# Optimization experiments

Hardware: AMD Instinct MI355X
Metric: run time of the kernel (lower is better)

## Reference

```python
import jax, jax.numpy as jnp
import numpy as np

NEG_SLOPE = 0.2  # PyG GATConv default


def gat_conv(x, edge_index, W, a_src, a_dst, bias):
    """Single-head PyG-style GATConv (eval mode, add_self_loops=True)."""
    N = x.shape[0]
    h = x @ W  # [N, F_out]
    # add self loops
    loops = jnp.arange(N, dtype=edge_index.dtype)
    src = jnp.concatenate([edge_index[0], loops])  # [E+N]
    dst = jnp.concatenate([edge_index[1], loops])
    # per-edge attention logits: a_src . h_j + a_dst . h_i  (j=src, i=dst)
    alpha_s = h @ a_src  # [N]
    alpha_d = h @ a_dst  # [N]
    e = jax.nn.leaky_relu(alpha_s[src] + alpha_d[dst], NEG_SLOPE)  # [E+N]
    # segment softmax over incoming edges of each dst node
    m = jax.ops.segment_max(e, dst, num_segments=N)
    ex = jnp.exp(e - m[dst])
    denom = jax.ops.segment_sum(ex, dst, num_segments=N)
    alpha = ex / denom[dst]  # [E+N]
    # weighted scatter-aggregate of source features
    out = jax.ops.segment_sum(h[src] * alpha[:, None], dst, num_segments=N)
    return out + bias


def setup_inputs() -> dict:
    key = jax.random.key(0)
    ks = jax.random.split(key, 12)
    N, E = 100000, 3200000
    Fin, H, Fout = 128, 32, 32
    x = jax.random.normal(ks[0], (N, Fin), dtype=jnp.float32)
    edge_index = jax.random.randint(ks[1], (2, E), 0, N, dtype=jnp.int64)
    s = 1.0 / np.sqrt(Fin)
    W1 = jax.random.uniform(ks[2], (Fin, H), jnp.float32, -s, s)
    a1s = jax.random.uniform(ks[3], (H,), jnp.float32, -s, s)
    a1d = jax.random.uniform(ks[4], (H,), jnp.float32, -s, s)
    b1 = jnp.zeros((H,), jnp.float32)
    s2 = 1.0 / np.sqrt(H)
    W2 = jax.random.uniform(ks[5], (H, H), jnp.float32, -s2, s2)
    a2s = jax.random.uniform(ks[6], (H,), jnp.float32, -s2, s2)
    a2d = jax.random.uniform(ks[7], (H,), jnp.float32, -s2, s2)
    b2 = jnp.zeros((H,), jnp.float32)
    Wf = jax.random.uniform(ks[8], (H, Fout), jnp.float32, -s2, s2)
    bf = jax.random.uniform(ks[9], (Fout,), jnp.float32, -s2, s2)
    return {"x": x, "edge_index": edge_index, "W1": W1, "a1s": a1s, "a1d": a1d,
            "b1": b1, "W2": W2, "a2s": a2s, "a2d": a2d, "b2": b2,
            "Wf": Wf, "bf": bf}


def reference(x, edge_index, W1, a1s, a1d, b1, W2, a2s, a2d, b2, Wf, bf):
    h = jax.nn.relu(gat_conv(x, edge_index, W1, a1s, a1d, b1))
    h = jax.nn.relu(gat_conv(h, edge_index, W2, a2s, a2d, b2))
    return h @ Wf + bf
```

## Files before the change

kernel.cpp:

```cpp
#include <hip/hip_runtime.h>

#define NEG_SLOPE 0.2f
#define BK_LOG 9
#define BK_NODES (1 << BK_LOG)
#define TILE_EPT 24
#define TILE_E (256 * TILE_EPT)

typedef __attribute__((ext_vector_type(8))) short bf8_t;
typedef __attribute__((ext_vector_type(4))) float f32x4;

__device__ __forceinline__ float leaky(float v) { return v > 0.0f ? v : NEG_SLOPE * v; }

__device__ __forceinline__ unsigned short f2bf(float f) {
    unsigned u = __float_as_uint(f);
    u += 0x7fffu + ((u >> 16) & 1u);
    return (unsigned short)(u >> 16);
}
__device__ __forceinline__ float bf2f(unsigned short h) {
    return __uint_as_float(((unsigned)h) << 16);
}

__device__ __forceinline__ int scan256_excl(int v, int* tmp) {
    int t = threadIdx.x;
    tmp[t] = v;
    __syncthreads();
    for (int d = 1; d < 256; d <<= 1) {
        int x = (t >= d) ? tmp[t - d] : 0;
        __syncthreads();
        tmp[t] += x;
        __syncthreads();
    }
    int r = tmp[t] - v;
    __syncthreads();
    return r;
}


__global__ __launch_bounds__(256) void k_bzero(int* __restrict__ bcnt) {
    bcnt[threadIdx.x] = 0;
}

__global__ __launch_bounds__(256) void k_bcount(const int* __restrict__ edst,
                                                int* __restrict__ bcnt, int E) {
    __shared__ int th[256];
    int t = threadIdx.x;
    th[t] = 0;
    __syncthreads();
    int base = blockIdx.x * TILE_E;
#pragma unroll
    for (int k = 0; k < TILE_EPT; ++k) {
        int e = base + t + k * 256;
        if (e < E) atomicAdd(&th[edst[e] >> BK_LOG], 1);
    }
    __syncthreads();
    if (th[t]) atomicAdd(&bcnt[t], th[t]);
}

__global__ __launch_bounds__(256) void k_bscan(const int* __restrict__ bcnt,
                                               int* __restrict__ bbase,
                                               int* __restrict__ bcur,
                                               int* __restrict__ off, int N, int E) {
    __shared__ int tmp[256];
    int t = threadIdx.x;
    int ex = scan256_excl(bcnt[t], tmp);
    bbase[t] = ex;
    bcur[t]  = ex;
    if (t == 0) { bbase[256] = E; off[N] = E; }
}

__global__ __launch_bounds__(256) void k_bplace(const int* __restrict__ esrc,
                                                const int* __restrict__ edst,
                                                int* __restrict__ bcur,
                                                unsigned* __restrict__ pairs, int E) {
    __shared__ int2 sp[TILE_E];
    __shared__ int th[256], tx[256], rb[256], tmp[256];
    int t = threadIdx.x;
    th[t] = 0;
    __syncthreads();
    int base = blockIdx.x * TILE_E;
    int tot  = min(TILE_E, E - base);
#pragma unroll
    for (int k = 0; k < TILE_EPT; ++k) {
        int e = base + t + k * 256;
        if (e < E) atomicAdd(&th[edst[e] >> BK_LOG], 1);
    }
    __syncthreads();
    int cnt = th[t];
    tx[t] = scan256_excl(cnt, tmp);
    rb[t] = atomicAdd(&bcur[t], cnt);
    th[t] = 0;
    __syncthreads();
#pragma unroll
    for (int k = 0; k < TILE_EPT; ++k) {
        int e = base + t + k * 256;
        if (e < E) {
            int s = esrc[e], d = edst[e];
            int b = d >> BK_LOG;
            int r = atomicAdd(&th[b], 1);
            sp[tx[b] + r] = make_int2(s, d);
        }
    }
    __syncthreads();
    for (int i = t; i < tot; i += 256) {
        int2 p = sp[i];
        int  b = p.y >> BK_LOG;
        pairs[rb[b] + (i - tx[b])] =
            ((unsigned)p.x << BK_LOG) | (unsigned)(p.y & (BK_NODES - 1));
    }
}

__global__ __launch_bounds__(512) void k_csr(const int* __restrict__ bbase,
                                             const unsigned* __restrict__ pairs,
                                             int* __restrict__ off,
                                             int* __restrict__ csr, int N) {
    __shared__ int lh[BK_NODES], lx[BK_NODES];
    int b = blockIdx.x, t = threadIdx.x;
    int lo = bbase[b], hi = bbase[b + 1];
    int node0 = b << BK_LOG;
    lh[t] = 0;
    __syncthreads();
    for (int j = lo + t; j < hi; j += 512)
        atomicAdd(&lh[pairs[j] & (BK_NODES - 1)], 1);
    __syncthreads();
    lx[t] = lh[t];
    __syncthreads();
    for (int d = 1; d < BK_NODES; d <<= 1) {
        int x0 = (t >= d) ? lx[t - d] : 0;
        __syncthreads();
        lx[t] += x0;
        __syncthreads();
    }
    lx[t] -= lh[t];
    if (node0 + t < N) off[node0 + t] = lo + lx[t];
    lh[t] = 0;
    __syncthreads();
    for (int j = lo + t; j < hi; j += 512) {
        unsigned p  = pairs[j];
        int      li = p & (BK_NODES - 1);
        int      r  = atomicAdd(&lh[li], 1);
        csr[lo + lx[li] + r] = (int)(p >> BK_LOG);
    }
}

__global__ __launch_bounds__(256) void k_wsplit(const float* __restrict__ W,
                                                unsigned short* __restrict__ wh,
                                                unsigned short* __restrict__ wl,
                                                int K) {
    int idx = blockIdx.x * 256 + threadIdx.x;
    int KT = K >> 5;
    if (idx >= KT * 128) return;
    int lane = idx & 63;
    int nt = (idx >> 6) & 1;
    int kt = idx >> 7;
    int q = lane >> 4, c = lane & 15;
#pragma unroll
    for (int j = 0; j < 8; ++j) {
        int k = kt * 32 + q * 8 + j;
        int n = nt * 16 + c;
        float w = W[k * 32 + n];
        unsigned short hi = f2bf(w);
        wh[idx * 8 + j] = hi;
        wl[idx * 8 + j] = f2bf(w - bf2f(hi));
    }
}

template <int FIN, bool ATT>
__global__ __launch_bounds__(256) void gemm_mfma(
    const float* __restrict__ x,
    const unsigned short* __restrict__ wh, const unsigned short* __restrict__ wl,
    const float* __restrict__ a_s, const float* __restrict__ a_d,
    const float* __restrict__ bias,
    float* __restrict__ h, float* __restrict__ alpha_s,
    float* __restrict__ alpha_d, int N)
{
    constexpr int KT = FIN / 32;
    int lane = threadIdx.x & 63;
    int mt   = blockIdx.x * 4 + (threadIdx.x >> 6);
    int m0   = mt * 16;
    if (m0 >= N) return;
    int q = lane >> 4, c = lane & 15;

    bf8_t Bh[KT][2], Bl[KT][2];
#pragma unroll
    for (int kt = 0; kt < KT; ++kt)
#pragma unroll
        for (int nt = 0; nt < 2; ++nt) {
            Bh[kt][nt] = *(const bf8_t*)(wh + ((size_t)(kt * 2 + nt) * 64 + lane) * 8);
            Bl[kt][nt] = *(const bf8_t*)(wl + ((size_t)(kt * 2 + nt) * 64 + lane) * 8);
        }

    int rowa = m0 + c;
    if (rowa >= N) rowa = N - 1;
    const float* xr = x + (size_t)rowa * FIN;
    bf8_t Ah[KT], Al[KT];
#pragma unroll
    for (int kt = 0; kt < KT; ++kt) {
        f32x4 v0 = *(const f32x4*)(xr + kt * 32 + q * 8);
        f32x4 v1 = *(const f32x4*)(xr + kt * 32 + q * 8 + 4);
#pragma unroll
        for (int j = 0; j < 8; ++j) {
            float f = (j < 4) ? v0[j] : v1[j - 4];
            unsigned short hi = f2bf(f);
            Ah[kt][j] = (short)hi;
            Al[kt][j] = (short)f2bf(f - bf2f(hi));
        }
    }

    f32x4 acc0 = {0.f, 0.f, 0.f, 0.f}, acc1 = {0.f, 0.f, 0.f, 0.f};
#pragma unroll
    for (int kt = 0; kt < KT; ++kt) {
        acc0 = __builtin_amdgcn_mfma_f32_16x16x32_bf16(Ah[kt], Bh[kt][0], acc0, 0, 0, 0);
        acc1 = __builtin_amdgcn_mfma_f32_16x16x32_bf16(Ah[kt], Bh[kt][1], acc1, 0, 0, 0);
        acc0 = __builtin_amdgcn_mfma_f32_16x16x32_bf16(Al[kt], Bh[kt][0], acc0, 0, 0, 0);
        acc1 = __builtin_amdgcn_mfma_f32_16x16x32_bf16(Al[kt], Bh[kt][1], acc1, 0, 0, 0);
        acc0 = __builtin_amdgcn_mfma_f32_16x16x32_bf16(Ah[kt], Bl[kt][0], acc0, 0, 0, 0);
        acc1 = __builtin_amdgcn_mfma_f32_16x16x32_bf16(Ah[kt], Bl[kt][1], acc1, 0, 0, 0);
    }

#pragma unroll
    for (int reg = 0; reg < 4; ++reg) {
        int r = m0 + q * 4 + reg;
        if (r < N) {
            float v0s = acc0[reg], v1s = acc1[reg];
            if (!ATT) { v0s += bias[c]; v1s += bias[c + 16]; }
            h[(size_t)r * 32 + c]      = v0s;
            h[(size_t)r * 32 + 16 + c] = v1s;
        }
    }
    if (ATT) {
        float as0 = a_s[c], as1 = a_s[c + 16];
        float ad0 = a_d[c], ad1 = a_d[c + 16];
#pragma unroll
        for (int reg = 0; reg < 4; ++reg) {
            float ps = acc0[reg] * as0 + acc1[reg] * as1;
            float pd = acc0[reg] * ad0 + acc1[reg] * ad1;
#pragma unroll
            for (int msk = 8; msk >= 1; msk >>= 1) {
                ps += __shfl_xor(ps, msk);
                pd += __shfl_xor(pd, msk);
            }
            int r = m0 + q * 4 + reg;
            if (c == 0 && r < N) {
                alpha_s[r] = ps;
                alpha_d[r] = pd;
            }
        }
    }
}

__global__ __launch_bounds__(256) void fused_agg(
    const int* __restrict__ csr, const int* __restrict__ off,
    const float* __restrict__ alpha_s, const float* __restrict__ alpha_d,
    const float* __restrict__ h, const float* __restrict__ bias,
    float* __restrict__ out, int N)
{
    int t = blockIdx.x * 256 + threadIdx.x;
    int i = t >> 3, q = t & 7;
    if (i >= N) return;
    int s0 = off[i], s1 = off[i + 1];
    float ad = alpha_d[i];

    const float* hq = h + q * 4;

    float w   = __expf(leaky(alpha_s[i] + ad));
    float den = w;
    f32x4 hv  = *(const f32x4*)(hq + (size_t)i * 32);
    f32x4 acc;
    acc[0] = w * hv[0]; acc[1] = w * hv[1]; acc[2] = w * hv[2]; acc[3] = w * hv[3];

    int j = s0;
    for (; j + 32 <= s1; j += 32) {
        int c0 = csr[j + q];
        int c1 = csr[j + 8 + q];
        int c2 = csr[j + 16 + q];
        int c3 = csr[j + 24 + q];
        float a0 = alpha_s[c0], a1 = alpha_s[c1], a2 = alpha_s[c2], a3 = alpha_s[c3];
        float w0 = __expf(leaky(a0 + ad));
        float w1 = __expf(leaky(a1 + ad));
        float w2 = __expf(leaky(a2 + ad));
        float w3 = __expf(leaky(a3 + ad));
        int o0 = c0 << 5, o1 = c1 << 5, o2 = c2 << 5, o3 = c3 << 5;
#pragma unroll
        for (int e = 0; e < 8; ++e) {
            int   e0 = __shfl(o0, e, 8); float f0 = __shfl(w0, e, 8);
            int   e1 = __shfl(o1, e, 8); float f1 = __shfl(w1, e, 8);
            int   e2 = __shfl(o2, e, 8); float f2 = __shfl(w2, e, 8);
            int   e3 = __shfl(o3, e, 8); float f3 = __shfl(w3, e, 8);
            f32x4 g0 = *(const f32x4*)(hq + e0);
            f32x4 g1 = *(const f32x4*)(hq + e1);
            f32x4 g2 = *(const f32x4*)(hq + e2);
            f32x4 g3 = *(const f32x4*)(hq + e3);
            den += (f0 + f1) + (f2 + f3);
            acc[0] += f0 * g0[0]; acc[1] += f0 * g0[1];
            acc[2] += f0 * g0[2]; acc[3] += f0 * g0[3];
            acc[0] += f1 * g1[0]; acc[1] += f1 * g1[1];
            acc[2] += f1 * g1[2]; acc[3] += f1 * g1[3];
            acc[0] += f2 * g2[0]; acc[1] += f2 * g2[1];
            acc[2] += f2 * g2[2]; acc[3] += f2 * g2[3];
            acc[0] += f3 * g3[0]; acc[1] += f3 * g3[1];
            acc[2] += f3 * g3[2]; acc[3] += f3 * g3[3];
        }
    }
    for (; j + 8 <= s1; j += 8) {
        int   c  = csr[j + q];
        float wv = __expf(leaky(alpha_s[c] + ad));
        int   co = c << 5;
#pragma unroll
        for (int e = 0; e < 8; ++e) {
            int   ce = __shfl(co, e, 8);
            float we = __shfl(wv, e, 8);
            f32x4 hg = *(const f32x4*)(hq + ce);
            den += we;
            acc[0] += we * hg[0]; acc[1] += we * hg[1];
            acc[2] += we * hg[2]; acc[3] += we * hg[3];
        }
    }
    int rem = s1 - j;
    if (rem > 0) {
        int c = 0; float wv = 0.0f;
        if (q < rem) {
            c  = csr[j + q];
            wv = __expf(leaky(alpha_s[c] + ad));
        }
        int co = c << 5;
        for (int e = 0; e < rem; ++e) {
            int   ce = __shfl(co, e, 8);
            float we = __shfl(wv, e, 8);
            f32x4 hg = *(const f32x4*)(hq + ce);
            den += we;
            acc[0] += we * hg[0]; acc[1] += we * hg[1];
            acc[2] += we * hg[2]; acc[3] += we * hg[3];
        }
    }

    float inv = 1.0f / den;
    f32x4 b4  = *(const f32x4*)(bias + q * 4);
    f32x4 r;
    r[0] = fmaxf(acc[0] * inv + b4[0], 0.0f);
    r[1] = fmaxf(acc[1] * inv + b4[1], 0.0f);
    r[2] = fmaxf(acc[2] * inv + b4[2], 0.0f);
    r[3] = fmaxf(acc[3] * inv + b4[3], 0.0f);
    *(f32x4*)(out + (size_t)i * 32 + q * 4) = r;
}

extern "C" void kernel_launch(void* const* d_in, const int* in_sizes, int n_in,
                              void* d_out, int out_size, void* d_ws, size_t ws_size,
                              hipStream_t stream)
{
    const float* x   = (const float*)d_in[0];
    const int*   ei  = (const int*)d_in[1];
    const float* W1  = (const float*)d_in[2];
    const float* a1s = (const float*)d_in[3];
    const float* a1d = (const float*)d_in[4];
    const float* b1  = (const float*)d_in[5];
    const float* W2  = (const float*)d_in[6];
    const float* a2s = (const float*)d_in[7];
    const float* a2d = (const float*)d_in[8];
    const float* b2  = (const float*)d_in[9];
    const float* Wf  = (const float*)d_in[10];
    const float* bf  = (const float*)d_in[11];

    const int N = in_sizes[0] / 128;
    const int E = in_sizes[1] / 2;
    const int* esrc = ei;
    const int* edst = ei + E;
    const int B1 = (N + BK_NODES - 1) >> BK_LOG;

    float* ws = (float*)d_ws;
    float* h1      = ws;
    float* h2      = h1 + (size_t)N * 32;
    float* alpha_s = h2 + (size_t)N * 32;
    float* alpha_d = alpha_s + N;
    int*   off     = (int*)(alpha_d + N);
    int*   csr     = off + (N + 1);
    int*   bcnt    = csr + E;
    int*   bbase   = bcnt + 256;
    int*   bcur    = bbase + 257;
    unsigned short* wfb =
        (unsigned short*)(((uintptr_t)(bcur + 256) + 15) & ~(uintptr_t)15);
    unsigned short* wh1 = wfb;
    unsigned short* wl1 = wh1 + 4096;
    unsigned short* wh2 = wl1 + 4096;
    unsigned short* wl2 = wh2 + 1024;
    unsigned short* whf = wl2 + 1024;
    unsigned short* wlf = whf + 1024;
    unsigned* pairs = ((size_t)E <= (size_t)64 * N)
                          ? (unsigned*)h1
                          : (unsigned*)(wlf + 1024);

    const int nb_agg  = (N * 8 + 255) / 256;
    const int nb_tile = (E + TILE_E - 1) / TILE_E;
    const int nb_gemm = ((N + 15) / 16 + 3) / 4;

    k_wsplit<<<2, 256, 0, stream>>>(W1, wh1, wl1, 128);
    k_wsplit<<<1, 256, 0, stream>>>(W2, wh2, wl2, 32);
    k_wsplit<<<1, 256, 0, stream>>>(Wf, whf, wlf, 32);

    k_bzero  <<<1, 256, 0, stream>>>(bcnt);
    k_bcount <<<nb_tile, 256, 0, stream>>>(edst, bcnt, E);
    k_bscan  <<<1, 256, 0, stream>>>(bcnt, bbase, bcur, off, N, E);
    k_bplace <<<nb_tile, 256, 0, stream>>>(esrc, edst, bcur, pairs, E);
    k_csr    <<<B1, 512, 0, stream>>>(bbase, pairs, off, csr, N);

    gemm_mfma<128, true><<<nb_gemm, 256, 0, stream>>>(
        x, wh1, wl1, a1s, a1d, nullptr, h1, alpha_s, alpha_d, N);
    fused_agg<<<nb_agg, 256, 0, stream>>>(csr, off, alpha_s, alpha_d, h1, b1, h2, N);

    gemm_mfma<32, true><<<nb_gemm, 256, 0, stream>>>(
        h2, wh2, wl2, a2s, a2d, nullptr, h1, alpha_s, alpha_d, N);
    fused_agg<<<nb_agg, 256, 0, stream>>>(csr, off, alpha_s, alpha_d, h1, b2, h2, N);

    gemm_mfma<32, false><<<nb_gemm, 256, 0, stream>>>(
        h2, whf, wlf, nullptr, nullptr, bf, (float*)d_out, nullptr, nullptr, N);
}
```

Measured before the change: 353.3 us.

## Merge prep kernels and co-schedule layer-1 GEMM with edge bucket counting

Folds the three weight-split launches and the bucket-counter zeroing into one prep kernel. The layer-1 GEMM moves into the same launch as the bucket-count pass, so the compute-bound GEMM blocks can overlap the memory-bound counting blocks. The pairs scratch buffer moves from h1 to h2 so h1 survives the CSR build. The aggregation tail loops become a single predicated 32-wide loop, which removes branches but wastes lanes on low-degree nodes.

```diff
diff --git a/kernel.cpp b/kernel.cpp
--- a/kernel.cpp
+++ b/kernel.cpp
@@ -35,26 +35,166 @@
     return r;
 }
 
-
-__global__ __launch_bounds__(256) void k_bzero(int* __restrict__ bcnt) {
-    bcnt[threadIdx.x] = 0;
-}
-
-__global__ __launch_bounds__(256) void k_bcount(const int* __restrict__ edst,
-                                                int* __restrict__ bcnt, int E) {
-    __shared__ int th[256];
-    int t = threadIdx.x;
-    th[t] = 0;
-    __syncthreads();
-    int base = blockIdx.x * TILE_E;
-#pragma unroll
-    for (int k = 0; k < TILE_EPT; ++k) {
-        int e = base + t + k * 256;
-        if (e < E) atomicAdd(&th[edst[e] >> BK_LOG], 1);
-    }
-    __syncthreads();
-    if (th[t]) atomicAdd(&bcnt[t], th[t]);
-}
+__device__ __forceinline__ void wsplit_body(int blk, int tid,
+                                            const float* __restrict__ W,
+                                            unsigned short* __restrict__ wh,
+                                            unsigned short* __restrict__ wl, int K) {
+    int idx = blk * 256 + tid;
+    int KT = K >> 5;
+    if (idx >= KT * 128) return;
+    int lane = idx & 63;
+    int nt = (idx >> 6) & 1;
+    int kt = idx >> 7;
+    int q = lane >> 4, c = lane & 15;
+#pragma unroll
+    for (int j = 0; j < 8; ++j) {
+        int k = kt * 32 + q * 8 + j;
+        int n = nt * 16 + c;
+        float w = W[k * 32 + n];
+        unsigned short hi = f2bf(w);
+        wh[idx * 8 + j] = hi;
+        wl[idx * 8 + j] = f2bf(w - bf2f(hi));
+    }
+}
+
+__global__ __launch_bounds__(256) void k_prep(
+    const float* __restrict__ W1, unsigned short* __restrict__ wh1, unsigned short* __restrict__ wl1,
+    const float* __restrict__ W2, unsigned short* __restrict__ wh2, unsigned short* __restrict__ wl2,
+    const float* __restrict__ Wf, unsigned short* __restrict__ whf, unsigned short* __restrict__ wlf,
+    int* __restrict__ bcnt)
+{
+    int b = blockIdx.x, t = threadIdx.x;
+    if (b < 2)       wsplit_body(b, t, W1, wh1, wl1, 128);
+    else if (b == 2) wsplit_body(0, t, W2, wh2, wl2, 32);
+    else if (b == 3) wsplit_body(0, t, Wf, whf, wlf, 32);
+    else             bcnt[t] = 0;
+}
+
+template <int FIN, bool ATT>
+__device__ __forceinline__ void gemm_body(
+    int blk, int tid,
+    const float* __restrict__ x,
+    const unsigned short* __restrict__ wh, const unsigned short* __restrict__ wl,
+    const float* __restrict__ a_s, const float* __restrict__ a_d,
+    const float* __restrict__ bias,
+    float* __restrict__ h, float* __restrict__ alpha_s,
+    float* __restrict__ alpha_d, int N)
+{
+    constexpr int KT = FIN / 32;
+    int lane = tid & 63;
+    int mt   = blk * 4 + (tid >> 6);
+    int m0   = mt * 16;
+    if (m0 >= N) return;
+    int q = lane >> 4, c = lane & 15;
+
+    bf8_t Bh[KT][2], Bl[KT][2];
+#pragma unroll
+    for (int kt = 0; kt < KT; ++kt)
+#pragma unroll
+        for (int nt = 0; nt < 2; ++nt) {
+            Bh[kt][nt] = *(const bf8_t*)(wh + ((size_t)(kt * 2 + nt) * 64 + lane) * 8);
+            Bl[kt][nt] = *(const bf8_t*)(wl + ((size_t)(kt * 2 + nt) * 64 + lane) * 8);
+        }
+
+    int rowa = m0 + c;
+    if (rowa >= N) rowa = N - 1;
+    const float* xr = x + (size_t)rowa * FIN;
+    bf8_t Ah[KT], Al[KT];
+#pragma unroll
+    for (int kt = 0; kt < KT; ++kt) {
+        f32x4 v0 = *(const f32x4*)(xr + kt * 32 + q * 8);
+        f32x4 v1 = *(const f32x4*)(xr + kt * 32 + q * 8 + 4);
+#pragma unroll
+        for (int j = 0; j < 8; ++j) {
+            float f = (j < 4) ? v0[j] : v1[j - 4];
+            unsigned short hi = f2bf(f);
+            Ah[kt][j] = (short)hi;
+            Al[kt][j] = (short)f2bf(f - bf2f(hi));
+        }
+    }
+
+    f32x4 acc0 = {0.f, 0.f, 0.f, 0.f}, acc1 = {0.f, 0.f, 0.f, 0.f};
+#pragma unroll
+    for (int kt = 0; kt < KT; ++kt) {
+        acc0 = __builtin_amdgcn_mfma_f32_16x16x32_bf16(Ah[kt], Bh[kt][0], acc0, 0, 0, 0);
+        acc1 = __builtin_amdgcn_mfma_f32_16x16x32_bf16(Ah[kt], Bh[kt][1], acc1, 0, 0, 0);
+        acc0 = __builtin_amdgcn_mfma_f32_16x16x32_bf16(Al[kt], Bh[kt][0], acc0, 0, 0, 0);
+        acc1 = __builtin_amdgcn_mfma_f32_16x16x32_bf16(Al[kt], Bh[kt][1], acc1, 0, 0, 0);
+        acc0 = __builtin_amdgcn_mfma_f32_16x16x32_bf16(Ah[kt], Bl[kt][0], acc0, 0, 0, 0);
+        acc1 = __builtin_amdgcn_mfma_f32_16x16x32_bf16(Ah[kt], Bl[kt][1], acc1, 0, 0, 0);
+    }
+
+#pragma unroll
+    for (int reg = 0; reg < 4; ++reg) {
+        int r = m0 + q * 4 + reg;
+        if (r < N) {
+            float v0s = acc0[reg], v1s = acc1[reg];
+            if (!ATT) { v0s += bias[c]; v1s += bias[c + 16]; }
+            h[(size_t)r * 32 + c]      = v0s;
+            h[(size_t)r * 32 + 16 + c] = v1s;
+        }
+    }
+    if (ATT) {
+        float as0 = a_s[c], as1 = a_s[c + 16];
+        float ad0 = a_d[c], ad1 = a_d[c + 16];
+#pragma unroll
+        for (int reg = 0; reg < 4; ++reg) {
+            float ps = acc0[reg] * as0 + acc1[reg] * as1;
+            float pd = acc0[reg] * ad0 + acc1[reg] * ad1;
+#pragma unroll
+            for (int msk = 8; msk >= 1; msk >>= 1) {
+                ps += __shfl_xor(ps, msk);
+                pd += __shfl_xor(pd, msk);
+            }
+            int r = m0 + q * 4 + reg;
+            if (c == 0 && r < N) {
+                alpha_s[r] = ps;
+                alpha_d[r] = pd;
+            }
+        }
+    }
+}
+
+template <int FIN, bool ATT>
+__global__ __launch_bounds__(256) void gemm_mfma(
+    const float* __restrict__ x,
+    const unsigned short* __restrict__ wh, const unsigned short* __restrict__ wl,
+    const float* __restrict__ a_s, const float* __restrict__ a_d,
+    const float* __restrict__ bias,
+    float* __restrict__ h, float* __restrict__ alpha_s,
+    float* __restrict__ alpha_d, int N)
+{
+    gemm_body<FIN, ATT>(blockIdx.x, threadIdx.x, x, wh, wl, a_s, a_d, bias,
+                        h, alpha_s, alpha_d, N);
+}
+
+__global__ __launch_bounds__(256) void k_bcount_gemm1(
+    const int* __restrict__ edst, int* __restrict__ bcnt, int E, int nb_tile,
+    const float* __restrict__ x,
+    const unsigned short* __restrict__ wh, const unsigned short* __restrict__ wl,
+    const float* __restrict__ a_s, const float* __restrict__ a_d,
+    float* __restrict__ h, float* __restrict__ alpha_s,
+    float* __restrict__ alpha_d, int N)
+{
+    if ((int)blockIdx.x < nb_tile) {
+        __shared__ int th[256];
+        int t = threadIdx.x;
+        th[t] = 0;
+        __syncthreads();
+        int base = blockIdx.x * TILE_E;
+#pragma unroll
+        for (int k = 0; k < TILE_EPT; ++k) {
+            int e = base + t + k * 256;
+            if (e < E) atomicAdd(&th[edst[e] >> BK_LOG], 1);
+        }
+        __syncthreads();
+        if (th[t]) atomicAdd(&bcnt[t], th[t]);
+    } else {
+        gemm_body<128, true>(blockIdx.x - nb_tile, threadIdx.x, x, wh, wl,
+                             a_s, a_d, nullptr, h, alpha_s, alpha_d, N);
+    }
+}
+
 
 __global__ __launch_bounds__(256) void k_bscan(const int* __restrict__ bcnt,
                                                int* __restrict__ bbase,
@@ -142,112 +282,6 @@
     }
 }
 
-__global__ __launch_bounds__(256) void k_wsplit(const float* __restrict__ W,
-                                                unsigned short* __restrict__ wh,
-                                                unsigned short* __restrict__ wl,
-                                                int K) {
-    int idx = blockIdx.x * 256 + threadIdx.x;
-    int KT = K >> 5;
-    if (idx >= KT * 128) return;
-    int lane = idx & 63;
-    int nt = (idx >> 6) & 1;
-    int kt = idx >> 7;
-    int q = lane >> 4, c = lane & 15;
-#pragma unroll
-    for (int j = 0; j < 8; ++j) {
-        int k = kt * 32 + q * 8 + j;
-        int n = nt * 16 + c;
-        float w = W[k * 32 + n];
-        unsigned short hi = f2bf(w);
-        wh[idx * 8 + j] = hi;
-        wl[idx * 8 + j] = f2bf(w - bf2f(hi));
-    }
-}
-
-template <int FIN, bool ATT>
-__global__ __launch_bounds__(256) void gemm_mfma(
-    const float* __restrict__ x,
-    const unsigned short* __restrict__ wh, const unsigned short* __restrict__ wl,
-    const float* __restrict__ a_s, const float* __restrict__ a_d,
-    const float* __restrict__ bias,
-    float* __restrict__ h, float* __restrict__ alpha_s,
-    float* __restrict__ alpha_d, int N)
-{
-    constexpr int KT = FIN / 32;
-    int lane = threadIdx.x & 63;
-    int mt   = blockIdx.x * 4 + (threadIdx.x >> 6);
-    int m0   = mt * 16;
-    if (m0 >= N) return;
-    int q = lane >> 4, c = lane & 15;
-
-    bf8_t Bh[KT][2], Bl[KT][2];
-#pragma unroll
-    for (int kt = 0; kt < KT; ++kt)
-#pragma unroll
-        for (int nt = 0; nt < 2; ++nt) {
-            Bh[kt][nt] = *(const bf8_t*)(wh + ((size_t)(kt * 2 + nt) * 64 + lane) * 8);
-            Bl[kt][nt] = *(const bf8_t*)(wl + ((size_t)(kt * 2 + nt) * 64 + lane) * 8);
-        }
-
-    int rowa = m0 + c;
-    if (rowa >= N) rowa = N - 1;
-    const float* xr = x + (size_t)rowa * FIN;
-    bf8_t Ah[KT], Al[KT];
-#pragma unroll
-    for (int kt = 0; kt < KT; ++kt) {
-        f32x4 v0 = *(const f32x4*)(xr + kt * 32 + q * 8);
-        f32x4 v1 = *(const f32x4*)(xr + kt * 32 + q * 8 + 4);
-#pragma unroll
-        for (int j = 0; j < 8; ++j) {
-            float f = (j < 4) ? v0[j] : v1[j - 4];
-            unsigned short hi = f2bf(f);
-            Ah[kt][j] = (short)hi;
-            Al[kt][j] = (short)f2bf(f - bf2f(hi));
-        }
-    }
-
-    f32x4 acc0 = {0.f, 0.f, 0.f, 0.f}, acc1 = {0.f, 0.f, 0.f, 0.f};
-#pragma unroll
-    for (int kt = 0; kt < KT; ++kt) {
-        acc0 = __builtin_amdgcn_mfma_f32_16x16x32_bf16(Ah[kt], Bh[kt][0], acc0, 0, 0, 0);
-        acc1 = __builtin_amdgcn_mfma_f32_16x16x32_bf16(Ah[kt], Bh[kt][1], acc1, 0, 0, 0);
-        acc0 = __builtin_amdgcn_mfma_f32_16x16x32_bf16(Al[kt], Bh[kt][0], acc0, 0, 0, 0);
-        acc1 = __builtin_amdgcn_mfma_f32_16x16x32_bf16(Al[kt], Bh[kt][1], acc1, 0, 0, 0);
-        acc0 = __builtin_amdgcn_mfma_f32_16x16x32_bf16(Ah[kt], Bl[kt][0], acc0, 0, 0, 0);
-        acc1 = __builtin_amdgcn_mfma_f32_16x16x32_bf16(Ah[kt], Bl[kt][1], acc1, 0, 0, 0);
-    }
-
-#pragma unroll
-    for (int reg = 0; reg < 4; ++reg) {
-        int r = m0 + q * 4 + reg;
-        if (r < N) {
-            float v0s = acc0[reg], v1s = acc1[reg];
-            if (!ATT) { v0s += bias[c]; v1s += bias[c + 16]; }
-            h[(size_t)r * 32 + c]      = v0s;
-            h[(size_t)r * 32 + 16 + c] = v1s;
-        }
-    }
-    if (ATT) {
-        float as0 = a_s[c], as1 = a_s[c + 16];
-        float ad0 = a_d[c], ad1 = a_d[c + 16];
-#pragma unroll
-        for (int reg = 0; reg < 4; ++reg) {
-            float ps = acc0[reg] * as0 + acc1[reg] * as1;
-            float pd = acc0[reg] * ad0 + acc1[reg] * ad1;
-#pragma unroll
-            for (int msk = 8; msk >= 1; msk >>= 1) {
-                ps += __shfl_xor(ps, msk);
-                pd += __shfl_xor(pd, msk);
-            }
-            int r = m0 + q * 4 + reg;
-            if (c == 0 && r < N) {
-                alpha_s[r] = ps;
-                alpha_d[r] = pd;
-            }
-        }
-    }
-}
-
 __global__ __launch_bounds__(256) void fused_agg(
     const int* __restrict__ csr, const int* __restrict__ off,
     const float* __restrict__ alpha_s, const float* __restrict__ alpha_d,
@@ -268,17 +302,20 @@
     f32x4 acc;
     acc[0] = w * hv[0]; acc[1] = w * hv[1]; acc[2] = w * hv[2]; acc[3] = w * hv[3];
 
-    int j = s0;
-    for (; j + 32 <= s1; j += 32) {
-        int c0 = csr[j + q];
-        int c1 = csr[j + 8 + q];
-        int c2 = csr[j + 16 + q];
-        int c3 = csr[j + 24 + q];
-        float a0 = alpha_s[c0], a1 = alpha_s[c1], a2 = alpha_s[c2], a3 = alpha_s[c3];
-        float w0 = __expf(leaky(a0 + ad));
-        float w1 = __expf(leaky(a1 + ad));
-        float w2 = __expf(leaky(a2 + ad));
-        float w3 = __expf(leaky(a3 + ad));
+    for (int j = s0; j < s1; j += 32) {
+        int i0 = j + q, i1 = i0 + 8, i2 = i0 + 16, i3 = i0 + 24;
+        int c0 = (i0 < s1) ? csr[i0] : 0;
+        int c1 = (i1 < s1) ? csr[i1] : 0;
+        int c2 = (i2 < s1) ? csr[i2] : 0;
+        int c3 = (i3 < s1) ? csr[i3] : 0;
+        float e0x = __expf(leaky(alpha_s[c0] + ad));
+        float e1x = __expf(leaky(alpha_s[c1] + ad));
+        float e2x = __expf(leaky(alpha_s[c2] + ad));
+        float e3x = __expf(leaky(alpha_s[c3] + ad));
+        float w0 = (i0 < s1) ? e0x : 0.0f;
+        float w1 = (i1 < s1) ? e1x : 0.0f;
+        float w2 = (i2 < s1) ? e2x : 0.0f;
+        float w3 = (i3 < s1) ? e3x : 0.0f;
         int o0 = c0 << 5, o1 = c1 << 5, o2 = c2 << 5, o3 = c3 << 5;
 #pragma unroll
         for (int e = 0; e < 8; ++e) {
@@ -301,37 +338,6 @@
             acc[2] += f3 * g3[2]; acc[3] += f3 * g3[3];
         }
     }
-    for (; j + 8 <= s1; j += 8) {
-        int   c  = csr[j + q];
-        float wv = __expf(leaky(alpha_s[c] + ad));
-        int   co = c << 5;
-#pragma unroll
-        for (int e = 0; e < 8; ++e) {
-            int   ce = __shfl(co, e, 8);
-            float we = __shfl(wv, e, 8);
-            f32x4 hg = *(const f32x4*)(hq + ce);
-            den += we;
-            acc[0] += we * hg[0]; acc[1] += we * hg[1];
-            acc[2] += we * hg[2]; acc[3] += we * hg[3];
-        }
-    }
-    int rem = s1 - j;
-    if (rem > 0) {
-        int c = 0; float wv = 0.0f;
-        if (q < rem) {
-            c  = csr[j + q];
-            wv = __expf(leaky(alpha_s[c] + ad));
-        }
-        int co = c << 5;
-        for (int e = 0; e < rem; ++e) {
-            int   ce = __shfl(co, e, 8);
-            float we = __shfl(wv, e, 8);
-            f32x4 hg = *(const f32x4*)(hq + ce);
-            den += we;
-            acc[0] += we * hg[0]; acc[1] += we * hg[1];
-            acc[2] += we * hg[2]; acc[3] += we * hg[3];
-        }
-    }
 
     float inv = 1.0f / den;
     f32x4 b4  = *(const f32x4*)(bias + q * 4);
@@ -384,26 +390,23 @@
     unsigned short* wl2 = wh2 + 1024;
     unsigned short* whf = wl2 + 1024;
     unsigned short* wlf = whf + 1024;
-    unsigned* pairs = ((size_t)E <= (size_t)64 * N)
-                          ? (unsigned*)h1
+    unsigned* pairs = ((size_t)E <= (size_t)32 * N)
+                          ? (unsigned*)h2
                           : (unsigned*)(wlf + 1024);
 
     const int nb_agg  = (N * 8 + 255) / 256;
     const int nb_tile = (E + TILE_E - 1) / TILE_E;
     const int nb_gemm = ((N + 15) / 16 + 3) / 4;
 
-    k_wsplit<<<2, 256, 0, stream>>>(W1, wh1, wl1, 128);
-    k_wsplit<<<1, 256, 0, stream>>>(W2, wh2, wl2, 32);
-    k_wsplit<<<1, 256, 0, stream>>>(Wf, whf, wlf, 32);
-
-    k_bzero  <<<1, 256, 0, stream>>>(bcnt);
-    k_bcount <<<nb_tile, 256, 0, stream>>>(edst, bcnt, E);
+    k_prep<<<5, 256, 0, stream>>>(W1, wh1, wl1, W2, wh2, wl2, Wf, whf, wlf, bcnt);
+
+    k_bcount_gemm1<<<nb_tile + nb_gemm, 256, 0, stream>>>(
+        edst, bcnt, E, nb_tile, x, wh1, wl1, a1s, a1d, h1, alpha_s, alpha_d, N);
+
     k_bscan  <<<1, 256, 0, stream>>>(bcnt, bbase, bcur, off, N, E);
     k_bplace <<<nb_tile, 256, 0, stream>>>(esrc, edst, bcur, pairs, E);
     k_csr    <<<B1, 512, 0, stream>>>(bbase, pairs, off, csr, N);
 
-    gemm_mfma<128, true><<<nb_gemm, 256, 0, stream>>>(
-        x, wh1, wl1, a1s, a1d, nullptr, h1, alpha_s, alpha_d, N);
     fused_agg<<<nb_agg, 256, 0, stream>>>(csr, off, alpha_s, alpha_d, h1, b1, h2, N);
 
     gemm_mfma<32, true><<<nb_gemm, 256, 0, stream>>>(
```

Measured after the change: 339.0 us. 1.04x faster.
